# Kernel optimization log

Hardware: AMD Instinct MI355X
Metric: run time of the kernel (lower is better)

## Reference

```python
import jax, jax.numpy as jnp
import numpy as np

D_MODEL = 1024
NUM_HEADS = 16
D_K = D_MODEL // NUM_HEADS
THETA = 10000.0


def apply_rope(x, positions):
    # x: [BH, S, d_k], positions: [S] int
    half = D_K // 2
    inv_freq = THETA ** (-jnp.arange(0, half, dtype=jnp.float32) / half)  # [half]
    ang = positions.astype(jnp.float32)[:, None] * inv_freq[None, :]       # [S, half]
    cos, sin = jnp.cos(ang), jnp.sin(ang)
    x1 = x[..., 0::2]  # [BH, S, half]
    x2 = x[..., 1::2]
    r1 = x1 * cos - x2 * sin
    r2 = x1 * sin + x2 * cos
    # interleave back: [..., half, 2] -> [..., d_k]
    return jnp.stack([r1, r2], axis=-1).reshape(x.shape)


def setup_inputs() -> dict:
    key = jax.random.key(0)
    ks = jax.random.split(key, 5)
    B, S = 4, 2048
    scale = 1.0 / np.sqrt(D_MODEL)
    return {
        "x": jax.random.normal(ks[0], (B, S, D_MODEL), dtype=jnp.float32),
        "token_positions": jnp.arange(S, dtype=jnp.int32),
        "Wq": jax.random.normal(ks[1], (D_MODEL, D_MODEL), dtype=jnp.float32) * scale,
        "Wk": jax.random.normal(ks[2], (D_MODEL, D_MODEL), dtype=jnp.float32) * scale,
        "Wv": jax.random.normal(ks[3], (D_MODEL, D_MODEL), dtype=jnp.float32) * scale,
        "Wo": jax.random.normal(ks[4], (D_MODEL, D_MODEL), dtype=jnp.float32) * scale,
    }


def reference(x, token_positions, Wq, Wk, Wv, Wo):
    B, S, D = x.shape
    H, dk = NUM_HEADS, D_K

    def split_heads(t):
        # [B, S, D] -> [B*H, S, dk]
        return t.reshape(B, S, H, dk).transpose(0, 2, 1, 3).reshape(B * H, S, dk)

    q = split_heads(x @ Wq.T)
    k = split_heads(x @ Wk.T)
    v = split_heads(x @ Wv.T)

    q = apply_rope(q, token_positions)
    k = apply_rope(k, token_positions)

    scores = jnp.einsum('bqd,bkd->bqk', q, k) / jnp.sqrt(jnp.float32(dk))
    causal = jnp.tril(jnp.ones((S, S), dtype=bool))
    scores = jnp.where(causal[None], scores, jnp.finfo(scores.dtype).min)
    attn = jax.nn.softmax(scores, axis=-1)
    out = jnp.einsum('bqk,bkd->bqd', attn, v)  # [B*H, S, dk]

    out = out.reshape(B, H, S, dk).transpose(0, 2, 1, 3).reshape(B, S, D)
    return out @ Wo.T
```

## Files before the change

### kernel.cpp

```cpp
#include <hip/hip_runtime.h>
#include <hip/hip_bf16.h>
#include <math.h>

#define D_MODEL 1024
#define NHEAD   16
#define DKH     64
#define BATCH   4
#define SEQ     2048
#define BH      (BATCH*NHEAD)
#define MROWS   (BATCH*SEQ)

typedef __attribute__((ext_vector_type(8))) short bf16x8;
typedef __attribute__((ext_vector_type(4))) short bf16x4;
typedef __attribute__((ext_vector_type(4))) float f32x4;

__device__ __forceinline__ short f2bf(float x){
    union { float f; unsigned u; } v; v.f = x;
    unsigned r = (v.u + 0x7fffu + ((v.u >> 16) & 1u)) >> 16;
    return (short)r;
}
__device__ __forceinline__ float bf2f(short s){
    union { unsigned u; float f; } v; v.u = ((unsigned)(unsigned short)s) << 16; return v.f;
}
__device__ __forceinline__ unsigned fasu(float x){ union{float f;unsigned u;} v; v.f=x; return v.u; }
__device__ __forceinline__ float uasf(unsigned x){ union{unsigned u;float f;} v; v.u=x; return v.f; }
__device__ __forceinline__ f32x4 mfma16(bf16x8 a, bf16x8 b, f32x4 c){
    return __builtin_amdgcn_mfma_f32_16x16x32_bf16(a, b, c, 0, 0, 0);
}

__device__ __forceinline__ void split4(float4 f, uint2* hi, uint2* lo){
    unsigned u0=fasu(f.x), u1=fasu(f.y), u2=fasu(f.z), u3=fasu(f.w);
    unsigned h0=u0&0xFFFF0000u, h1=u1&0xFFFF0000u, h2=u2&0xFFFF0000u, h3=u3&0xFFFF0000u;
    float l0=f.x-uasf(h0), l1=f.y-uasf(h1), l2=f.z-uasf(h2), l3=f.w-uasf(h3);
    hi->x = h1 | (u0>>16);
    hi->y = h3 | (u2>>16);
    unsigned v0=fasu(l0), v1=fasu(l1), v2=fasu(l2), v3=fasu(l3);
    lo->x = (v1&0xFFFF0000u) | (v0>>16);
    lo->y = (v3&0xFFFF0000u) | (v2>>16);
}

__global__ __launch_bounds__(256, 2)
void gemm_qkv_kernel(const float* __restrict__ x,
                     const int*   __restrict__ pos,
                     const float* __restrict__ Wq,
                     const float* __restrict__ Wk,
                     const float* __restrict__ Wv,
                     float* __restrict__ qb,
                     float* __restrict__ kb,
                     float* __restrict__ vb)
{
    const int which = blockIdx.z;
    const float* __restrict__ W    = (which==0)?Wq:(which==1)?Wk:Wv;
    float*       __restrict__ outb = (which==0)?qb:(which==1)?kb:vb;

    __shared__ short lAh[128*64], lAl[128*64], lBh[128*64], lBl[128*64];

    const int t  = threadIdx.x;
    const int w  = t >> 6, l = t & 63;
    const int ln = l & 15, g = l >> 4;
    const int wr = w >> 1, wc = w & 1;
    const int m0 = blockIdx.x * 128, n0 = blockIdx.y * 128;

    f32x4 acc[4][4];
    #pragma unroll
    for (int mi=0;mi<4;mi++)
        #pragma unroll
        for (int ni=0;ni<4;ni++) acc[mi][ni] = (f32x4){0.f,0.f,0.f,0.f};

    for (int k0 = 0; k0 < D_MODEL; k0 += 64){
        __syncthreads();
        #pragma unroll
        for (int i=0;i<8;i++){
            int c    = i*256 + t;
            int row  = c >> 4;
            int col4 = (c & 15) << 2;
            int si   = (row*64 + col4) ^ ((row & 7) << 3);
            float4 fa = *(const float4*)&x[(size_t)(m0+row)*D_MODEL + k0 + col4];
            uint2 ah_, al_;
            split4(fa, &ah_, &al_);
            *(uint2*)&lAh[si] = ah_;
            *(uint2*)&lAl[si] = al_;
            float4 fb = *(const float4*)&W[(size_t)(n0+row)*D_MODEL + k0 + col4];
            uint2 bh_, bl_;
            split4(fb, &bh_, &bl_);
            *(uint2*)&lBh[si] = bh_;
            *(uint2*)&lBl[si] = bl_;
        }
        __syncthreads();

        #pragma unroll
        for (int ks=0; ks<2; ks++){
            bf16x8 ah[4], al[4], bh[4], bl[4];
            #pragma unroll
            for (int mi=0;mi<4;mi++){
                int row = wr*64 + mi*16 + ln;
                int si  = (row*64 + ks*32 + g*8) ^ ((row & 7) << 3);
                ah[mi] = *(const bf16x8*)&lAh[si];
                al[mi] = *(const bf16x8*)&lAl[si];
            }
            #pragma unroll
            for (int ni=0;ni<4;ni++){
                int row = wc*64 + ni*16 + ln;
                int si  = (row*64 + ks*32 + g*8) ^ ((row & 7) << 3);
                bh[ni] = *(const bf16x8*)&lBh[si];
                bl[ni] = *(const bf16x8*)&lBl[si];
            }
            #pragma unroll
            for (int mi=0;mi<4;mi++)
                #pragma unroll
                for (int ni=0;ni<4;ni++){
                    acc[mi][ni] = mfma16(ah[mi], bh[ni], acc[mi][ni]);
                    acc[mi][ni] = mfma16(ah[mi], bl[ni], acc[mi][ni]);
                    acc[mi][ni] = mfma16(al[mi], bh[ni], acc[mi][ni]);
                }
        }
    }

    #pragma unroll
    for (int mi=0;mi<4;mi++){
        #pragma unroll
        for (int ni=0;ni<4;ni++){
            const int n  = n0 + wc*64 + ni*16 + ln;
            const int h  = n >> 6;
            const int cc = n & 63;
            float invf = 0.f;
            if (which < 2){
                const int j = cc >> 1;
                invf = __expf(-(float)j * 0.2878231366242557f);
            }
            #pragma unroll
            for (int r=0;r<4;r++){
                const int m = m0 + wr*64 + mi*16 + g*4 + r;
                const int b = m >> 11;
                const int s = m & 2047;
                float v = acc[mi][ni][r];
                float p = __shfl_xor(v, 1);
                float res;
                if (which < 2){
                    float ang = (float)pos[s] * invf;
                    float sn, cs; __sincosf(ang, &sn, &cs);
                    res = ((n & 1) == 0) ? (v*cs - p*sn) : (p*sn + v*cs);
                } else {
                    res = v;
                }
                outb[(((size_t)(b*NHEAD + h))*SEQ + s)*DKH + cc] = res;
            }
        }
    }
}

__global__ __launch_bounds__(256)
void flash_mfma_kernel(const float* __restrict__ qb,
                       const float* __restrict__ kb,
                       const float* __restrict__ vb,
                       float* __restrict__ ob)
{
    const int qt = (int)(gridDim.x - 1) - (int)blockIdx.x;
    const int bh = blockIdx.y;
    const int t  = threadIdx.x;
    const int w  = t >> 6;
    const int l  = t & 63;
    const int ln = l & 15;
    const int g  = l >> 4;

    __shared__ short lKhi[4096], lKlo[4096];
    __shared__ short lVhi[4096], lVlo[4096];
    __shared__ short lPhi[4][2048], lPlo[4][2048];

    const int swz = (ln & 7) << 3;

    bf16x8 qh[2][2], ql[2][2];
    {
        const int qrow0 = qt*128 + w*32;
        #pragma unroll
        for (int rt=0; rt<2; rt++){
            #pragma unroll
            for (int ks=0; ks<2; ks++){
                const float* qp = qb + ((size_t)bh*SEQ + qrow0 + rt*16 + ln)*DKH + ks*32 + g*8;
                float4 x0 = *(const float4*)qp;
                float4 x1 = *(const float4*)(qp+4);
                float xs[8] = {x0.x,x0.y,x0.z,x0.w,x1.x,x1.y,x1.z,x1.w};
                short hi[8], lo[8];
                #pragma unroll
                for (int i=0;i<8;i++){
                    float v = xs[i]*0.125f;
                    hi[i] = f2bf(v);
                    lo[i] = f2bf(v - bf2f(hi[i]));
                }
                qh[rt][ks] = (bf16x8){hi[0],hi[1],hi[2],hi[3],hi[4],hi[5],hi[6],hi[7]};
                ql[rt][ks] = (bf16x8){lo[0],lo[1],lo[2],lo[3],lo[4],lo[5],lo[6],lo[7]};
            }
        }
    }

    f32x4 oacc[2][4];
    #pragma unroll
    for (int rt=0; rt<2; rt++)
        #pragma unroll
        for (int dm=0; dm<4; dm++)
            oacc[rt][dm] = (f32x4){0.f,0.f,0.f,0.f};
    float m_run[2] = {-3.0e38f, -3.0e38f};
    float l_run[2] = {0.f, 0.f};

    const int ktmax = 2*qt + 1;
    for (int kt = 0; kt <= ktmax; ++kt){
        __syncthreads();

        #pragma unroll
        for (int rep=0; rep<4; rep++){
            int idx = t + rep*256;
            int row = idx >> 4;
            int kc  = (idx & 15) << 2;
            float4 kx = *(const float4*)&kb[((size_t)bh*SEQ + kt*64 + row)*DKH + kc];
            float xs[4] = {kx.x,kx.y,kx.z,kx.w};
            short hi[4], lo[4];
            #pragma unroll
            for (int i=0;i<4;i++){
                hi[i] = f2bf(xs[i]);
                lo[i] = f2bf(xs[i] - bf2f(hi[i]));
            }
            int si = (row*64 + kc) ^ ((row&7)<<3);
            *(bf16x4*)&lKhi[si] = (bf16x4){hi[0],hi[1],hi[2],hi[3]};
            *(bf16x4*)&lKlo[si] = (bf16x4){lo[0],lo[1],lo[2],lo[3]};
        }
        {
            int d  = t & 63;
            int c0 = (t >> 6) << 4;
            const float* vcol = vb + ((size_t)bh*SEQ + kt*64 + c0)*DKH + d;
            float vvf[16];
            #pragma unroll
            for (int j=0;j<16;j++) vvf[j] = vcol[(size_t)j*DKH];
            short hh[16], ll[16];
            #pragma unroll
            for (int j=0;j<16;j++){
                hh[j] = f2bf(vvf[j]);
                ll[j] = f2bf(vvf[j] - bf2f(hh[j]));
            }
            int si0 = (d*64 + c0)     ^ ((d&7)<<3);
            int si1 = (d*64 + c0 + 8) ^ ((d&7)<<3);
            *(bf16x8*)&lVhi[si0] = (bf16x8){hh[0],hh[1],hh[2],hh[3],hh[4],hh[5],hh[6],hh[7]};
            *(bf16x8*)&lVhi[si1] = (bf16x8){hh[8],hh[9],hh[10],hh[11],hh[12],hh[13],hh[14],hh[15]};
            *(bf16x8*)&lVlo[si0] = (bf16x8){ll[0],ll[1],ll[2],ll[3],ll[4],ll[5],ll[6],ll[7]};
            *(bf16x8*)&lVlo[si1] = (bf16x8){ll[8],ll[9],ll[10],ll[11],ll[12],ll[13],ll[14],ll[15]};
        }
        __syncthreads();

        if (kt*64 > qt*128 + w*32 + 31) continue;

        f32x4 s[4][2];
        #pragma unroll
        for (int cm=0; cm<4; cm++)
            #pragma unroll
            for (int rn=0; rn<2; rn++)
                s[cm][rn] = (f32x4){0.f,0.f,0.f,0.f};

        #pragma unroll
        for (int ks=0; ks<2; ks++){
            #pragma unroll
            for (int cm=0; cm<4; cm++){
                int si = ((cm*16 + ln)*64 + ks*32 + g*8) ^ swz;
                bf16x8 ah = *(const bf16x8*)&lKhi[si];
                bf16x8 al = *(const bf16x8*)&lKlo[si];
                #pragma unroll
                for (int rn=0; rn<2; rn++){
                    s[cm][rn] = mfma16(ah, qh[rn][ks], s[cm][rn]);
                    s[cm][rn] = mfma16(ah, ql[rn][ks], s[cm][rn]);
                    s[cm][rn] = mfma16(al, qh[rn][ks], s[cm][rn]);
                }
            }
        }

        if (kt*64 + 63 > qt*128 + w*32){
            #pragma unroll
            for (int cm=0; cm<4; cm++){
                #pragma unroll
                for (int rn=0; rn<2; rn++){
                    #pragma unroll
                    for (int r=0; r<4; r++){
                        int cg = kt*64 + cm*16 + g*4 + r;
                        int rg = qt*128 + w*32 + rn*16 + ln;
                        if (cg > rg) s[cm][rn][r] = -3.0e38f;
                    }
                }
            }
        }

        float alpha[2];
        #pragma unroll
        for (int rn=0; rn<2; rn++){
            float mx = -3.0e38f;
            #pragma unroll
            for (int cm=0; cm<4; cm++)
                #pragma unroll
                for (int r=0; r<4; r++) mx = fmaxf(mx, s[cm][rn][r]);
            mx = fmaxf(mx, __shfl_xor(mx, 16));
            mx = fmaxf(mx, __shfl_xor(mx, 32));
            float mnew = fmaxf(m_run[rn], mx);
            alpha[rn] = __expf(m_run[rn] - mnew);
            m_run[rn] = mnew;
            float ls = 0.f;
            #pragma unroll
            for (int cm=0; cm<4; cm++){
                #pragma unroll
                for (int r=0; r<4; r++){
                    float p = __expf(s[cm][rn][r] - mnew);
                    s[cm][rn][r] = p;
                    ls += p;
                }
            }
            ls += __shfl_xor(ls, 16);
            ls += __shfl_xor(ls, 32);
            l_run[rn] = l_run[rn]*alpha[rn] + ls;
        }

        #pragma unroll
        for (int rn=0; rn<2; rn++){
            #pragma unroll
            for (int cm=0; cm<4; cm++){
                short hi[4], lo[4];
                #pragma unroll
                for (int r=0; r<4; r++){
                    float p = s[cm][rn][r];
                    hi[r] = f2bf(p);
                    lo[r] = f2bf(p - bf2f(hi[r]));
                }
                int row = rn*16 + ln;
                int si = (row*64 + cm*16 + g*4) ^ ((row&7)<<3);
                *(bf16x4*)&lPhi[w][si] = (bf16x4){hi[0],hi[1],hi[2],hi[3]};
                *(bf16x4*)&lPlo[w][si] = (bf16x4){lo[0],lo[1],lo[2],lo[3]};
            }
        }

        #pragma unroll
        for (int rt=0; rt<2; rt++){
            #pragma unroll
            for (int r=0; r<4; r++){
                float a = __shfl(alpha[rt], g*4 + r);
                #pragma unroll
                for (int dm=0; dm<4; dm++) oacc[rt][dm][r] *= a;
            }
        }

        #pragma unroll
        for (int ks2=0; ks2<2; ks2++){
            bf16x8 ph[2], pl[2], vh[4], vl[4];
            #pragma unroll
            for (int rt=0; rt<2; rt++){
                int si = ((rt*16 + ln)*64 + ks2*32 + g*8) ^ swz;
                ph[rt] = *(const bf16x8*)&lPhi[w][si];
                pl[rt] = *(const bf16x8*)&lPlo[w][si];
            }
            #pragma unroll
            for (int dm=0; dm<4; dm++){
                int si = ((dm*16 + ln)*64 + ks2*32 + g*8) ^ swz;
                vh[dm] = *(const bf16x8*)&lVhi[si];
                vl[dm] = *(const bf16x8*)&lVlo[si];
            }
            #pragma unroll
            for (int rt=0; rt<2; rt++){
                #pragma unroll
                for (int dm=0; dm<4; dm++){
                    oacc[rt][dm] = mfma16(ph[rt], vh[dm], oacc[rt][dm]);
                    oacc[rt][dm] = mfma16(ph[rt], vl[dm], oacc[rt][dm]);
                    oacc[rt][dm] = mfma16(pl[rt], vh[dm], oacc[rt][dm]);
                }
            }
        }
    }

    #pragma unroll
    for (int rt=0; rt<2; rt++){
        float inv[4];
        #pragma unroll
        for (int r=0; r<4; r++) inv[r] = 1.0f / __shfl(l_run[rt], g*4 + r);
        #pragma unroll
        for (int dm=0; dm<4; dm++){
            #pragma unroll
            for (int r=0; r<4; r++){
                ob[((size_t)bh*SEQ + qt*128 + w*32 + rt*16 + g*4 + r)*DKH + dm*16 + ln]
                    = oacc[rt][dm][r] * inv[r];
            }
        }
    }
}

__global__ __launch_bounds__(256, 2)
void gemm_out_kernel(const float* __restrict__ ao,
                     const float* __restrict__ Wo,
                     float* __restrict__ out)
{
    __shared__ short lAh[128*64], lAl[128*64], lBh[128*64], lBl[128*64];

    const int t  = threadIdx.x;
    const int w  = t >> 6, l = t & 63;
    const int ln = l & 15, g = l >> 4;
    const int wr = w >> 1, wc = w & 1;
    const int m0 = blockIdx.x * 128, n0 = blockIdx.y * 128;

    f32x4 acc[4][4];
    #pragma unroll
    for (int mi=0;mi<4;mi++)
        #pragma unroll
        for (int ni=0;ni<4;ni++) acc[mi][ni] = (f32x4){0.f,0.f,0.f,0.f};

    for (int k0 = 0; k0 < D_MODEL; k0 += 64){
        const int hh = k0 >> 6;
        __syncthreads();
        #pragma unroll
        for (int i=0;i<8;i++){
            int c    = i*256 + t;
            int row  = c >> 4;
            int col4 = (c & 15) << 2;
            int si   = (row*64 + col4) ^ ((row & 7) << 3);
            const int m = m0 + row;
            const int b = m >> 11;
            const int s = m & 2047;
            float4 fa = *(const float4*)&ao[(((size_t)(b*NHEAD + hh))*SEQ + s)*DKH + col4];
            uint2 ah_, al_;
            split4(fa, &ah_, &al_);
            *(uint2*)&lAh[si] = ah_;
            *(uint2*)&lAl[si] = al_;
            float4 fb = *(const float4*)&Wo[(size_t)(n0+row)*D_MODEL + k0 + col4];
            uint2 bh_, bl_;
            split4(fb, &bh_, &bl_);
            *(uint2*)&lBh[si] = bh_;
            *(uint2*)&lBl[si] = bl_;
        }
        __syncthreads();

        #pragma unroll
        for (int ks=0; ks<2; ks++){
            bf16x8 ah[4], al[4], bh[4], bl[4];
            #pragma unroll
            for (int mi=0;mi<4;mi++){
                int row = wr*64 + mi*16 + ln;
                int si  = (row*64 + ks*32 + g*8) ^ ((row & 7) << 3);
                ah[mi] = *(const bf16x8*)&lAh[si];
                al[mi] = *(const bf16x8*)&lAl[si];
            }
            #pragma unroll
            for (int ni=0;ni<4;ni++){
                int row = wc*64 + ni*16 + ln;
                int si  = (row*64 + ks*32 + g*8) ^ ((row & 7) << 3);
                bh[ni] = *(const bf16x8*)&lBh[si];
                bl[ni] = *(const bf16x8*)&lBl[si];
            }
            #pragma unroll
            for (int mi=0;mi<4;mi++)
                #pragma unroll
                for (int ni=0;ni<4;ni++){
                    acc[mi][ni] = mfma16(ah[mi], bh[ni], acc[mi][ni]);
                    acc[mi][ni] = mfma16(ah[mi], bl[ni], acc[mi][ni]);
                    acc[mi][ni] = mfma16(al[mi], bh[ni], acc[mi][ni]);
                }
        }
    }

    #pragma unroll
    for (int mi=0;mi<4;mi++){
        #pragma unroll
        for (int ni=0;ni<4;ni++){
            const int n = n0 + wc*64 + ni*16 + ln;
            #pragma unroll
            for (int r=0;r<4;r++){
                const int m = m0 + wr*64 + mi*16 + g*4 + r;
                out[(size_t)m*D_MODEL + n] = acc[mi][ni][r];
            }
        }
    }
}

extern "C" void kernel_launch(void* const* d_in, const int* in_sizes, int n_in,
                              void* d_out, int out_size, void* d_ws, size_t ws_size,
                              hipStream_t stream)
{
    (void)in_sizes; (void)n_in; (void)out_size; (void)ws_size;
    const float* x   = (const float*)d_in[0];
    const int*   pos = (const int*)  d_in[1];
    const float* Wq  = (const float*)d_in[2];
    const float* Wk  = (const float*)d_in[3];
    const float* Wv  = (const float*)d_in[4];
    const float* Wo  = (const float*)d_in[5];
    float* out = (float*)d_out;

    const size_t per = (size_t)BH*SEQ*DKH;
    float* qb = (float*)d_ws;
    float* kb = qb + per;
    float* vb = kb + per;
    float* ao = qb;

    dim3 gA(MROWS/128, D_MODEL/128, 3);
    gemm_qkv_kernel<<<gA, 256, 0, stream>>>(x, pos, Wq, Wk, Wv, qb, kb, vb);

    dim3 gB(SEQ/128, BH);
    flash_mfma_kernel<<<gB, 256, 0, stream>>>(qb, kb, vb, ao);

    dim3 gC(MROWS/128, D_MODEL/128);
    gemm_out_kernel<<<gC, 256, 0, stream>>>(ao, Wo, out);
}
```

Measured before the change: 808.3 us.

## Halve K-tile and P buffers to shrink LDS and raise occupancy across kernels

```diff
diff --git a/kernel.cpp b/kernel.cpp
--- a/kernel.cpp
+++ b/kernel.cpp
@@ -39,7 +39,7 @@
     lo->y = (v3&0xFFFF0000u) | (v2>>16);
 }
 
-__global__ __launch_bounds__(256, 2)
+__global__ __launch_bounds__(256, 4)
 void gemm_qkv_kernel(const float* __restrict__ x,
                      const int*   __restrict__ pos,
                      const float* __restrict__ Wq,
@@ -53,7 +53,7 @@
     const float* __restrict__ W    = (which==0)?Wq:(which==1)?Wk:Wv;
     float*       __restrict__ outb = (which==0)?qb:(which==1)?kb:vb;
 
-    __shared__ short lAh[128*64], lAl[128*64], lBh[128*64], lBl[128*64];
+    __shared__ short lAh[128*32], lAl[128*32], lBh[128*32], lBl[128*32];
 
     const int t  = threadIdx.x;
     const int w  = t >> 6, l = t & 63;
@@ -67,14 +67,14 @@
         #pragma unroll
         for (int ni=0;ni<4;ni++) acc[mi][ni] = (f32x4){0.f,0.f,0.f,0.f};
 
-    for (int k0 = 0; k0 < D_MODEL; k0 += 64){
-        __syncthreads();
-        #pragma unroll
-        for (int i=0;i<8;i++){
+    for (int k0 = 0; k0 < D_MODEL; k0 += 32){
+        __syncthreads();
+        #pragma unroll
+        for (int i=0;i<4;i++){
             int c    = i*256 + t;
-            int row  = c >> 4;
-            int col4 = (c & 15) << 2;
-            int si   = (row*64 + col4) ^ ((row & 7) << 3);
+            int row  = c >> 3;
+            int col4 = (c & 7) << 2;
+            int si   = (row*32 + col4) ^ ((row & 7) << 3);
             float4 fa = *(const float4*)&x[(size_t)(m0+row)*D_MODEL + k0 + col4];
             uint2 ah_, al_;
             split4(fa, &ah_, &al_);
@@ -88,32 +88,29 @@
         }
         __syncthreads();
 
-        #pragma unroll
-        for (int ks=0; ks<2; ks++){
-            bf16x8 ah[4], al[4], bh[4], bl[4];
-            #pragma unroll
-            for (int mi=0;mi<4;mi++){
-                int row = wr*64 + mi*16 + ln;
-                int si  = (row*64 + ks*32 + g*8) ^ ((row & 7) << 3);
-                ah[mi] = *(const bf16x8*)&lAh[si];
-                al[mi] = *(const bf16x8*)&lAl[si];
-            }
+        bf16x8 ah[4], al[4], bh[4], bl[4];
+        #pragma unroll
+        for (int mi=0;mi<4;mi++){
+            int row = wr*64 + mi*16 + ln;
+            int si  = (row*32 + g*8) ^ ((row & 7) << 3);
+            ah[mi] = *(const bf16x8*)&lAh[si];
+            al[mi] = *(const bf16x8*)&lAl[si];
+        }
+        #pragma unroll
+        for (int ni=0;ni<4;ni++){
+            int row = wc*64 + ni*16 + ln;
+            int si  = (row*32 + g*8) ^ ((row & 7) << 3);
+            bh[ni] = *(const bf16x8*)&lBh[si];
+            bl[ni] = *(const bf16x8*)&lBl[si];
+        }
+        #pragma unroll
+        for (int mi=0;mi<4;mi++)
             #pragma unroll
             for (int ni=0;ni<4;ni++){
-                int row = wc*64 + ni*16 + ln;
-                int si  = (row*64 + ks*32 + g*8) ^ ((row & 7) << 3);
-                bh[ni] = *(const bf16x8*)&lBh[si];
-                bl[ni] = *(const bf16x8*)&lBl[si];
-            }
-            #pragma unroll
-            for (int mi=0;mi<4;mi++)
-                #pragma unroll
-                for (int ni=0;ni<4;ni++){
-                    acc[mi][ni] = mfma16(ah[mi], bh[ni], acc[mi][ni]);
-                    acc[mi][ni] = mfma16(ah[mi], bl[ni], acc[mi][ni]);
-                    acc[mi][ni] = mfma16(al[mi], bh[ni], acc[mi][ni]);
-                }
-        }
+                acc[mi][ni] = mfma16(ah[mi], bh[ni], acc[mi][ni]);
+                acc[mi][ni] = mfma16(ah[mi], bl[ni], acc[mi][ni]);
+                acc[mi][ni] = mfma16(al[mi], bh[ni], acc[mi][ni]);
+            }
     }
 
     #pragma unroll
@@ -149,7 +146,7 @@
     }
 }
 
-__global__ __launch_bounds__(256)
+__global__ __launch_bounds__(256, 3)
 void flash_mfma_kernel(const float* __restrict__ qb,
                        const float* __restrict__ kb,
                        const float* __restrict__ vb,
@@ -165,7 +162,7 @@
 
     __shared__ short lKhi[4096], lKlo[4096];
     __shared__ short lVhi[4096], lVlo[4096];
-    __shared__ short lPhi[4][2048], lPlo[4][2048];
+    __shared__ short lPhi[4][1024], lPlo[4][1024];
 
     const int swz = (ln & 7) << 3;
 
@@ -314,24 +311,6 @@
         }
 
         #pragma unroll
-        for (int rn=0; rn<2; rn++){
-            #pragma unroll
-            for (int cm=0; cm<4; cm++){
-                short hi[4], lo[4];
-                #pragma unroll
-                for (int r=0; r<4; r++){
-                    float p = s[cm][rn][r];
-                    hi[r] = f2bf(p);
-                    lo[r] = f2bf(p - bf2f(hi[r]));
-                }
-                int row = rn*16 + ln;
-                int si = (row*64 + cm*16 + g*4) ^ ((row&7)<<3);
-                *(bf16x4*)&lPhi[w][si] = (bf16x4){hi[0],hi[1],hi[2],hi[3]};
-                *(bf16x4*)&lPlo[w][si] = (bf16x4){lo[0],lo[1],lo[2],lo[3]};
-            }
-        }
-
-        #pragma unroll
         for (int rt=0; rt<2; rt++){
             #pragma unroll
             for (int r=0; r<4; r++){
@@ -342,17 +321,36 @@
         }
 
         #pragma unroll
-        for (int ks2=0; ks2<2; ks2++){
+        for (int h=0; h<2; h++){
+            #pragma unroll
+            for (int rn=0; rn<2; rn++){
+                #pragma unroll
+                for (int cm2=0; cm2<2; cm2++){
+                    const int cm = h*2 + cm2;
+                    short hi[4], lo[4];
+                    #pragma unroll
+                    for (int r=0; r<4; r++){
+                        float p = s[cm][rn][r];
+                        hi[r] = f2bf(p);
+                        lo[r] = f2bf(p - bf2f(hi[r]));
+                    }
+                    int row = rn*16 + ln;
+                    int si = (row*32 + cm2*16 + g*4) ^ ((row&7)<<3);
+                    *(bf16x4*)&lPhi[w][si] = (bf16x4){hi[0],hi[1],hi[2],hi[3]};
+                    *(bf16x4*)&lPlo[w][si] = (bf16x4){lo[0],lo[1],lo[2],lo[3]};
+                }
+            }
             bf16x8 ph[2], pl[2], vh[4], vl[4];
             #pragma unroll
             for (int rt=0; rt<2; rt++){
-                int si = ((rt*16 + ln)*64 + ks2*32 + g*8) ^ swz;
+                int row = rt*16 + ln;
+                int si = (row*32 + g*8) ^ ((row&7)<<3);
                 ph[rt] = *(const bf16x8*)&lPhi[w][si];
                 pl[rt] = *(const bf16x8*)&lPlo[w][si];
             }
             #pragma unroll
             for (int dm=0; dm<4; dm++){
-                int si = ((dm*16 + ln)*64 + ks2*32 + g*8) ^ swz;
+                int si = ((dm*16 + ln)*64 + h*32 + g*8) ^ swz;
                 vh[dm] = *(const bf16x8*)&lVhi[si];
                 vl[dm] = *(const bf16x8*)&lVlo[si];
             }
@@ -384,12 +382,12 @@
     }
 }
 
-__global__ __launch_bounds__(256, 2)
+__global__ __launch_bounds__(256, 4)
 void gemm_out_kernel(const float* __restrict__ ao,
                      const float* __restrict__ Wo,
                      float* __restrict__ out)
 {
-    __shared__ short lAh[128*64], lAl[128*64], lBh[128*64], lBl[128*64];
+    __shared__ short lAh[128*32], lAl[128*32], lBh[128*32], lBl[128*32];
 
     const int t  = threadIdx.x;
     const int w  = t >> 6, l = t & 63;
@@ -403,19 +401,20 @@
         #pragma unroll
         for (int ni=0;ni<4;ni++) acc[mi][ni] = (f32x4){0.f,0.f,0.f,0.f};
 
-    for (int k0 = 0; k0 < D_MODEL; k0 += 64){
+    for (int k0 = 0; k0 < D_MODEL; k0 += 32){
         const int hh = k0 >> 6;
-        __syncthreads();
-        #pragma unroll
-        for (int i=0;i<8;i++){
+        const int kin = k0 & 63;
+        __syncthreads();
+        #pragma unroll
+        for (int i=0;i<4;i++){
             int c    = i*256 + t;
-            int row  = c >> 4;
-            int col4 = (c & 15) << 2;
-            int si   = (row*64 + col4) ^ ((row & 7) << 3);
+            int row  = c >> 3;
+            int col4 = (c & 7) << 2;
+            int si   = (row*32 + col4) ^ ((row & 7) << 3);
             const int m = m0 + row;
             const int b = m >> 11;
             const int s = m & 2047;
-            float4 fa = *(const float4*)&ao[(((size_t)(b*NHEAD + hh))*SEQ + s)*DKH + col4];
+            float4 fa = *(const float4*)&ao[(((size_t)(b*NHEAD + hh))*SEQ + s)*DKH + kin + col4];
             uint2 ah_, al_;
             split4(fa, &ah_, &al_);
             *(uint2*)&lAh[si] = ah_;
@@ -428,32 +427,29 @@
         }
         __syncthreads();
 
-        #pragma unroll
-        for (int ks=0; ks<2; ks++){
-            bf16x8 ah[4], al[4], bh[4], bl[4];
-            #pragma unroll
-            for (int mi=0;mi<4;mi++){
-                int row = wr*64 + mi*16 + ln;
-                int si  = (row*64 + ks*32 + g*8) ^ ((row & 7) << 3);
-                ah[mi] = *(const bf16x8*)&lAh[si];
-                al[mi] = *(const bf16x8*)&lAl[si];
-            }
+        bf16x8 ah[4], al[4], bh[4], bl[4];
+        #pragma unroll
+        for (int mi=0;mi<4;mi++){
+            int row = wr*64 + mi*16 + ln;
+            int si  = (row*32 + g*8) ^ ((row & 7) << 3);
+            ah[mi] = *(const bf16x8*)&lAh[si];
+            al[mi] = *(const bf16x8*)&lAl[si];
+        }
+        #pragma unroll
+        for (int ni=0;ni<4;ni++){
+            int row = wc*64 + ni*16 + ln;
+            int si  = (row*32 + g*8) ^ ((row & 7) << 3);
+            bh[ni] = *(const bf16x8*)&lBh[si];
+            bl[ni] = *(const bf16x8*)&lBl[si];
+        }
+        #pragma unroll
+        for (int mi=0;mi<4;mi++)
             #pragma unroll
             for (int ni=0;ni<4;ni++){
-                int row = wc*64 + ni*16 + ln;
-                int si  = (row*64 + ks*32 + g*8) ^ ((row & 7) << 3);
-                bh[ni] = *(const bf16x8*)&lBh[si];
-                bl[ni] = *(const bf16x8*)&lBl[si];
-            }
-            #pragma unroll
-            for (int mi=0;mi<4;mi++)
-                #pragma unroll
-                for (int ni=0;ni<4;ni++){
-                    acc[mi][ni] = mfma16(ah[mi], bh[ni], acc[mi][ni]);
-                    acc[mi][ni] = mfma16(ah[mi], bl[ni], acc[mi][ni]);
-                    acc[mi][ni] = mfma16(al[mi], bh[ni], acc[mi][ni]);
-                }
-        }
+                acc[mi][ni] = mfma16(ah[mi], bh[ni], acc[mi][ni]);
+                acc[mi][ni] = mfma16(ah[mi], bl[ni], acc[mi][ni]);
+                acc[mi][ni] = mfma16(al[mi], bh[ni], acc[mi][ni]);
+            }
     }
 
     #pragma unroll
```

Result: slower. 1.152 ms (+42.6%).
